# Performance work log

Hardware: AMD Instinct MI355X
Metric: run time of the kernel (lower is better)

The kernel has to match this reference:

```python
import jax, jax.numpy as jnp
import numpy as np

NUM_NODES = 128
BATCH = 32768
G_BASE = np.array([8.0, 8.0, 16.0, 8.0, 8.0, 4.0, 8.0, 8.0, 4.0, 4.0, 4.0, 8.0], dtype=np.float32)
T_BASE = np.array([0.02, 0.02, 0.16, 0.28], dtype=np.float32)


def setup_inputs() -> dict:
    key = jax.random.key(0)
    k1, k2, k3, k4, k5, k6 = jax.random.split(key, 6)
    x = jax.random.normal(k1, (BATCH, NUM_NODES * 8), dtype=jnp.float32)
    t = jnp.zeros((), dtype=jnp.float32)
    node_connectivity = jax.random.normal(k2, (NUM_NODES, NUM_NODES), dtype=jnp.float32) * 0.1
    # per-node gain/time-constant params (init values + small perturbation so grads are generic)
    G = jnp.asarray(G_BASE)[None, :] * (1.0 + 0.05 * jax.random.normal(k3, (NUM_NODES, 12), dtype=jnp.float32))
    T = jnp.asarray(T_BASE)[None, :] * (1.0 + 0.05 * jax.random.normal(k4, (NUM_NODES, 4), dtype=jnp.float32))
    adaptation = jnp.ones((NUM_NODES,), dtype=jnp.float32) + 0.1 * jax.random.normal(k5, (NUM_NODES,), dtype=jnp.float32)
    R = jnp.ones((NUM_NODES,), dtype=jnp.float32) + 0.1 * jax.random.normal(k6, (NUM_NODES,), dtype=jnp.float32)
    return {"t": t, "x": x, "node_connectivity": node_connectivity, "G": G, "T": T,
            "adaptation": adaptation, "R": R}


def reference(t, x, node_connectivity, G, T, adaptation, R):
    # x: [B, N*8] state; activation = sigmoid branch of FlexibleCMC
    B = x.shape[0]
    N = node_connectivity.shape[0]
    x = jnp.clip(x, -100.0, 100.0)
    xs = x.reshape(B, N, 8)  # [B, N, 8]
    # S = sigmoid(R*x) - sigmoid(0)  (sigmoid activation branch)
    S = jax.nn.sigmoid(R[None, :, None] * xs) - 0.5  # [B, N, 8]
    # message passing: mean activity of each node, weighted by connectivity (no self-loop)
    m = xs.mean(axis=-1)  # [B, N]
    C = node_connectivity * (1.0 - jnp.eye(N, dtype=node_connectivity.dtype))
    node_input = jnp.einsum('bj,ij->bi', m, C)  # [B, N]
    scale = jax.nn.sigmoid(adaptation) * 0.1  # [N]

    g = lambda k: G[:, k]  # [N], broadcasts against [B, N]
    u1 = -g(0) * S[..., 0] - g(2) * S[..., 4] - g(1) * S[..., 2] + node_input
    f1 = scale * (u1 - 2.0 * xs[..., 1] - xs[..., 0] / T[:, 0]) / T[:, 0]
    u3 = g(7) * S[..., 0] - g(6) * S[..., 2] - g(11) * S[..., 4] + node_input
    f3 = scale * (u3 - 2.0 * xs[..., 3] - xs[..., 2] / T[:, 1]) / T[:, 1]
    u5 = g(4) * S[..., 0] + g(5) * S[..., 6] - g(3) * S[..., 4] + g(10) * S[..., 2] + node_input
    f5 = scale * (u5 - 2.0 * xs[..., 5] - xs[..., 4] / T[:, 2]) / T[:, 2]
    u7 = -g(9) * S[..., 6] - g(8) * S[..., 4] + node_input
    f7 = scale * (u7 - 2.0 * xs[..., 7] - xs[..., 6] / T[:, 3]) / T[:, 3]
    f0 = scale * xs[..., 1]
    f2 = scale * xs[..., 3]
    f4 = scale * xs[..., 5]
    f6 = scale * xs[..., 7]
    f = jnp.stack([f0, f1, f2, f3, f4, f5, f6, f7], axis=-1)  # [B, N, 8]
    return f.reshape(B, N * 8)
```

## Files before the change

kernel.cpp:

```cpp
#include <hip/hip_runtime.h>

#define NNODES 128
#define BATCH  32768
#define BLOCK  256
#define ROWS_PER_CHUNK 16
#define NCHUNKS (BATCH / ROWS_PER_CHUNK)
#define GRID   512

__device__ __forceinline__ float sigmoidf_(float z) {
    return 1.0f / (1.0f + __expf(-z));
}

__device__ __forceinline__ float clipf_(float v) {
    return fminf(fmaxf(v, -100.0f), 100.0f);
}

__device__ __forceinline__ void node_update(const float* xs8, float ni,
                                            const float* gi, const float* invTi,
                                            float sci, float Ri, float* f8) {
    float S0 = sigmoidf_(Ri * xs8[0]) - 0.5f;
    float S2 = sigmoidf_(Ri * xs8[2]) - 0.5f;
    float S4 = sigmoidf_(Ri * xs8[4]) - 0.5f;
    float S6 = sigmoidf_(Ri * xs8[6]) - 0.5f;
    float u1 = ni - gi[0] * S0 - gi[1] * S2 - gi[2]  * S4;
    float u3 = ni + gi[7] * S0 - gi[6] * S2 - gi[11] * S4;
    float u5 = ni + gi[4] * S0 + gi[10] * S2 - gi[3] * S4 + gi[5] * S6;
    float u7 = ni - gi[8] * S4 - gi[9] * S6;
    f8[0] = sci * xs8[1];
    f8[1] = sci * (u1 - 2.0f * xs8[1] - xs8[0] * invTi[0]) * invTi[0];
    f8[2] = sci * xs8[3];
    f8[3] = sci * (u3 - 2.0f * xs8[3] - xs8[2] * invTi[1]) * invTi[1];
    f8[4] = sci * xs8[5];
    f8[5] = sci * (u5 - 2.0f * xs8[5] - xs8[4] * invTi[2]) * invTi[2];
    f8[6] = sci * xs8[7];
    f8[7] = sci * (u7 - 2.0f * xs8[7] - xs8[6] * invTi[3]) * invTi[3];
}

__global__ __launch_bounds__(BLOCK, 2)
void cmc_kernel(const float* __restrict__ x,
                const float* __restrict__ C,
                const float* __restrict__ G,
                const float* __restrict__ T,
                const float* __restrict__ adap,
                const float* __restrict__ R,
                float* __restrict__ out)
{
    __shared__ float ct[NNODES * NNODES];
    __shared__ float m_lds[ROWS_PER_CHUNK][NNODES];

    const int tid    = threadIdx.x;
    const int lane31 = tid & 31;
    const int lr     = tid >> 5;
    const int n0     = lane31 * 4;

    {
        const int j4 = lane31 * 4;
        #pragma unroll
        for (int ii = 0; ii < 16; ++ii) {
            int i = lr + ii * 8;
            float4 c = *reinterpret_cast<const float4*>(C + i * NNODES + j4);
            if (i == j4 + 0) c.x = 0.0f;
            if (i == j4 + 1) c.y = 0.0f;
            if (i == j4 + 2) c.z = 0.0f;
            if (i == j4 + 3) c.w = 0.0f;
            float cv[4] = {c.x, c.y, c.z, c.w};
            #pragma unroll
            for (int k = 0; k < 4; ++k) {
                int j  = j4 + k;
                int sw = ((j >> 2) & 7) << 2;
                ct[j * NNODES + (i ^ sw)] = cv[k];
            }
        }
    }

    float g[4][12], invT[4][4], sc[4], Rr[4];
    #pragma unroll
    for (int i = 0; i < 4; ++i) {
        int n = n0 + i;
        #pragma unroll
        for (int k = 0; k < 12; ++k) g[i][k] = G[n * 12 + k];
        #pragma unroll
        for (int k = 0; k < 4; ++k) invT[i][k] = 1.0f / T[n * 4 + k];
        sc[i] = 0.1f * sigmoidf_(adap[n]);
        Rr[i] = R[n];
    }

    __syncthreads();

    for (int chunk = blockIdx.x; chunk < NCHUNKS; chunk += GRID) {
        const int r0 = chunk * ROWS_PER_CHUNK + lr;
        const int r1 = r0 + 8;

        float xv[2][32];
        {
            const float4* p0 = reinterpret_cast<const float4*>(x + (size_t)r0 * 1024 + n0 * 8);
            const float4* p1 = reinterpret_cast<const float4*>(x + (size_t)r1 * 1024 + n0 * 8);
            #pragma unroll
            for (int q = 0; q < 8; ++q) {
                float4 v = p0[q];
                xv[0][q * 4 + 0] = clipf_(v.x); xv[0][q * 4 + 1] = clipf_(v.y);
                xv[0][q * 4 + 2] = clipf_(v.z); xv[0][q * 4 + 3] = clipf_(v.w);
            }
            #pragma unroll
            for (int q = 0; q < 8; ++q) {
                float4 v = p1[q];
                xv[1][q * 4 + 0] = clipf_(v.x); xv[1][q * 4 + 1] = clipf_(v.y);
                xv[1][q * 4 + 2] = clipf_(v.z); xv[1][q * 4 + 3] = clipf_(v.w);
            }
        }

        {
            float4 ma, mb;
            float* pa = &ma.x; float* pb = &mb.x;
            #pragma unroll
            for (int i = 0; i < 4; ++i) {
                float s0 = 0.0f, s1 = 0.0f;
                #pragma unroll
                for (int k = 0; k < 8; ++k) { s0 += xv[0][i * 8 + k]; s1 += xv[1][i * 8 + k]; }
                pa[i] = s0 * 0.125f; pb[i] = s1 * 0.125f;
            }
            *reinterpret_cast<float4*>(&m_lds[lr][n0])     = ma;
            *reinterpret_cast<float4*>(&m_lds[lr + 8][n0]) = mb;
        }

        __syncthreads();

        float acc0[4] = {0, 0, 0, 0}, acc1[4] = {0, 0, 0, 0};
        #pragma unroll 8
        for (int j4 = 0; j4 < 32; ++j4) {
            float4 mA = *reinterpret_cast<const float4*>(&m_lds[lr][j4 * 4]);
            float4 mB = *reinterpret_cast<const float4*>(&m_lds[lr + 8][j4 * 4]);
            const float* pmA = &mA.x; const float* pmB = &mB.x;
            const int col = n0 ^ ((j4 & 7) << 2);
            #pragma unroll
            for (int c2 = 0; c2 < 4; ++c2) {
                int j = j4 * 4 + c2;
                float4 ct4 = *reinterpret_cast<const float4*>(&ct[j * NNODES + col]);
                float mv0 = pmA[c2], mv1 = pmB[c2];
                acc0[0] = fmaf(mv0, ct4.x, acc0[0]);
                acc0[1] = fmaf(mv0, ct4.y, acc0[1]);
                acc0[2] = fmaf(mv0, ct4.z, acc0[2]);
                acc0[3] = fmaf(mv0, ct4.w, acc0[3]);
                acc1[0] = fmaf(mv1, ct4.x, acc1[0]);
                acc1[1] = fmaf(mv1, ct4.y, acc1[1]);
                acc1[2] = fmaf(mv1, ct4.z, acc1[2]);
                acc1[3] = fmaf(mv1, ct4.w, acc1[3]);
            }
        }

        {
            float* o0 = out + (size_t)r0 * 1024 + n0 * 8;
            float* o1 = out + (size_t)r1 * 1024 + n0 * 8;
            #pragma unroll
            for (int i = 0; i < 4; ++i) {
                float f8[8];
                node_update(&xv[0][i * 8], acc0[i], g[i], invT[i], sc[i], Rr[i], f8);
                *reinterpret_cast<float4*>(o0 + i * 8)     = make_float4(f8[0], f8[1], f8[2], f8[3]);
                *reinterpret_cast<float4*>(o0 + i * 8 + 4) = make_float4(f8[4], f8[5], f8[6], f8[7]);
            }
            #pragma unroll
            for (int i = 0; i < 4; ++i) {
                float f8[8];
                node_update(&xv[1][i * 8], acc1[i], g[i], invT[i], sc[i], Rr[i], f8);
                *reinterpret_cast<float4*>(o1 + i * 8)     = make_float4(f8[0], f8[1], f8[2], f8[3]);
                *reinterpret_cast<float4*>(o1 + i * 8 + 4) = make_float4(f8[4], f8[5], f8[6], f8[7]);
            }
        }

        __syncthreads();
    }
}

extern "C" void kernel_launch(void* const* d_in, const int* in_sizes, int n_in,
                              void* d_out, int out_size, void* d_ws, size_t ws_size,
                              hipStream_t stream) {
    const float* x    = (const float*)d_in[1];
    const float* C    = (const float*)d_in[2];
    const float* G    = (const float*)d_in[3];
    const float* T    = (const float*)d_in[4];
    const float* adap = (const float*)d_in[5];
    const float* R    = (const float*)d_in[6];
    float* out        = (float*)d_out;

    hipLaunchKernelGGL(cmc_kernel, dim3(GRID), dim3(BLOCK), 0, stream,
                       x, C, G, T, adap, R, out);
}
```

Before: 77.10 us.

## Store connectivity in LDS as bf16, drop barriers, double occupancy

The transposed connectivity matrix is now kept in shared memory as bf16 instead of fp32, halving its LDS footprint. That allows four blocks per CU, so the grid grows to 1024 and the launch bounds change to match. The per-chunk __syncthreads are removed, relying on each m_lds row being written and read only by threads of the same wavefront. The aim is more waves in flight to hide memory latency in this bandwidth-bound kernel, at the cost of bf16 rounding error in node_input and a reliance on implicit wave-level ordering.

```diff
diff --git a/kernel.cpp b/kernel.cpp
--- a/kernel.cpp
+++ b/kernel.cpp
@@ -5,7 +5,7 @@
 #define BLOCK  256
 #define ROWS_PER_CHUNK 16
 #define NCHUNKS (BATCH / ROWS_PER_CHUNK)
-#define GRID   512
+#define GRID   1024
 
 __device__ __forceinline__ float sigmoidf_(float z) {
     return 1.0f / (1.0f + __expf(-z));
@@ -13,6 +13,11 @@
 
 __device__ __forceinline__ float clipf_(float v) {
     return fminf(fmaxf(v, -100.0f), 100.0f);
+}
+
+__device__ __forceinline__ unsigned short bf16_(float f) {
+    unsigned u = __float_as_uint(f);
+    return (unsigned short)((u + 0x8000u) >> 16);
 }
 
 __device__ __forceinline__ void node_update(const float* xs8, float ni,
@@ -36,7 +41,7 @@
     f8[7] = sci * (u7 - 2.0f * xs8[7] - xs8[6] * invTi[3]) * invTi[3];
 }
 
-__global__ __launch_bounds__(BLOCK, 2)
+__global__ __launch_bounds__(BLOCK, 4)
 void cmc_kernel(const float* __restrict__ x,
                 const float* __restrict__ C,
                 const float* __restrict__ G,
@@ -45,7 +50,7 @@
                 const float* __restrict__ R,
                 float* __restrict__ out)
 {
-    __shared__ float ct[NNODES * NNODES];
+    __shared__ unsigned short ct16[NNODES * NNODES];
     __shared__ float m_lds[ROWS_PER_CHUNK][NNODES];
 
     const int tid    = threadIdx.x;
@@ -54,21 +59,25 @@
     const int n0     = lane31 * 4;
 
     {
-        const int j4 = lane31 * 4;
+        const int j0 = (tid & 31) * 4;
+        const int tb = tid >> 5;
         #pragma unroll
-        for (int ii = 0; ii < 16; ++ii) {
-            int i = lr + ii * 8;
-            float4 c = *reinterpret_cast<const float4*>(C + i * NNODES + j4);
-            if (i == j4 + 0) c.x = 0.0f;
-            if (i == j4 + 1) c.y = 0.0f;
-            if (i == j4 + 2) c.z = 0.0f;
-            if (i == j4 + 3) c.w = 0.0f;
-            float cv[4] = {c.x, c.y, c.z, c.w};
+        for (int it = 0; it < 4; ++it) {
+            const int i0 = (tb + it * 8) * 4;
+            float4 row[4];
+            #pragma unroll
+            for (int r = 0; r < 4; ++r)
+                row[r] = *reinterpret_cast<const float4*>(C + (size_t)(i0 + r) * NNODES + j0);
             #pragma unroll
             for (int k = 0; k < 4; ++k) {
-                int j  = j4 + k;
-                int sw = ((j >> 2) & 7) << 2;
-                ct[j * NNODES + (i ^ sw)] = cv[k];
+                const int j = j0 + k;
+                ushort4 w;
+                w.x = (i0 + 0 == j) ? (unsigned short)0 : bf16_((&row[0].x)[k]);
+                w.y = (i0 + 1 == j) ? (unsigned short)0 : bf16_((&row[1].x)[k]);
+                w.z = (i0 + 2 == j) ? (unsigned short)0 : bf16_((&row[2].x)[k]);
+                w.w = (i0 + 3 == j) ? (unsigned short)0 : bf16_((&row[3].x)[k]);
+                const int col = i0 ^ ((j & 15) << 2);
+                *reinterpret_cast<ushort4*>(&ct16[j * NNODES + col]) = w;
             }
         }
     }
@@ -123,28 +132,30 @@
             *reinterpret_cast<float4*>(&m_lds[lr + 8][n0]) = mb;
         }
 
-        __syncthreads();
-
         float acc0[4] = {0, 0, 0, 0}, acc1[4] = {0, 0, 0, 0};
         #pragma unroll 8
         for (int j4 = 0; j4 < 32; ++j4) {
             float4 mA = *reinterpret_cast<const float4*>(&m_lds[lr][j4 * 4]);
             float4 mB = *reinterpret_cast<const float4*>(&m_lds[lr + 8][j4 * 4]);
             const float* pmA = &mA.x; const float* pmB = &mB.x;
-            const int col = n0 ^ ((j4 & 7) << 2);
             #pragma unroll
             for (int c2 = 0; c2 < 4; ++c2) {
-                int j = j4 * 4 + c2;
-                float4 ct4 = *reinterpret_cast<const float4*>(&ct[j * NNODES + col]);
+                const int j = j4 * 4 + c2;
+                const int col = n0 ^ ((j & 15) << 2);
+                uint2 cu = *reinterpret_cast<const uint2*>(&ct16[j * NNODES + col]);
+                float cv0 = __uint_as_float(cu.x << 16);
+                float cv1 = __uint_as_float(cu.x & 0xffff0000u);
+                float cv2 = __uint_as_float(cu.y << 16);
+                float cv3 = __uint_as_float(cu.y & 0xffff0000u);
                 float mv0 = pmA[c2], mv1 = pmB[c2];
-                acc0[0] = fmaf(mv0, ct4.x, acc0[0]);
-                acc0[1] = fmaf(mv0, ct4.y, acc0[1]);
-                acc0[2] = fmaf(mv0, ct4.z, acc0[2]);
-                acc0[3] = fmaf(mv0, ct4.w, acc0[3]);
-                acc1[0] = fmaf(mv1, ct4.x, acc1[0]);
-                acc1[1] = fmaf(mv1, ct4.y, acc1[1]);
-                acc1[2] = fmaf(mv1, ct4.z, acc1[2]);
-                acc1[3] = fmaf(mv1, ct4.w, acc1[3]);
+                acc0[0] = fmaf(mv0, cv0, acc0[0]);
+                acc0[1] = fmaf(mv0, cv1, acc0[1]);
+                acc0[2] = fmaf(mv0, cv2, acc0[2]);
+                acc0[3] = fmaf(mv0, cv3, acc0[3]);
+                acc1[0] = fmaf(mv1, cv0, acc1[0]);
+                acc1[1] = fmaf(mv1, cv1, acc1[1]);
+                acc1[2] = fmaf(mv1, cv2, acc1[2]);
+                acc1[3] = fmaf(mv1, cv3, acc1[3]);
             }
         }
 
@@ -166,8 +177,6 @@
                 *reinterpret_cast<float4*>(o1 + i * 8 + 4) = make_float4(f8[4], f8[5], f8[6], f8[7]);
             }
         }
-
-        __syncthreads();
     }
 }
 
```

Measured after the change: 235.5 us. 3.05x slower.
